# Kernel tuning notes

Measured on AMD Instinct MI355X. Metric: run time of the kernel, lower is better.

Reference implementation:

```python
import jax, jax.numpy as jnp
import numpy as np

S, B, NIN = 64, 64, 64          # att_width (= target_seq_len), batch, num_input
H1, HB, H = 128, 128, 128       # first LSTM size, biLSTM hidden, att_hid
MLP = (1024, 512, 256, 128, 1)  # h1..h4, num_output


def _lstm_cell(x, h, c, Wih, Whh, b):
    # PyTorch gate order: i, f, g, o
    z = x @ Wih.T + h @ Whh.T + b
    i, f, g, o = jnp.split(z, 4, axis=-1)
    c = jax.nn.sigmoid(f) * c + jax.nn.sigmoid(i) * jnp.tanh(g)
    h = jax.nn.sigmoid(o) * jnp.tanh(c)
    return h, c


def _lstm_seq(xs, Wih, Whh, b, reverse=False):
    # xs: [S, B, in] -> hs: [S, B, H], final (h, c)
    h0 = jnp.zeros((xs.shape[1], Whh.shape[1]), xs.dtype)

    def step(carry, x):
        h, c = _lstm_cell(x, carry[0], carry[1], Wih, Whh, b)
        return (h, c), h

    (h, c), hs = jax.lax.scan(step, (h0, h0), xs, reverse=reverse)
    return hs, (h, c)


def _forward(input_seqs,
             lstm1_Wih, lstm1_Whh, lstm1_b,
             bi2f_Wih, bi2f_Whh, bi2f_b, bi2b_Wih, bi2b_Whh, bi2b_b,
             bi3f_Wih, bi3f_Whh, bi3f_b, bi3b_Wih, bi3b_Whh, bi3b_b,
             enc_Wih, enc_Whh, enc_b,
             dec_Wih, dec_Whh, dec_b,
             att_fc_W, att_w,
             W1_W, W1_b, W2_W, W2_b, W3_W, W3_b, W4_W, W4_b, out_W, out_b):
    # 1) one-directional LSTM
    x, _ = _lstm_seq(input_seqs, lstm1_Wih, lstm1_Whh, lstm1_b)
    # 2-3) two stacked bidirectional LSTMs
    f, _ = _lstm_seq(x, bi2f_Wih, bi2f_Whh, bi2f_b)
    bk, _ = _lstm_seq(x, bi2b_Wih, bi2b_Whh, bi2b_b, reverse=True)
    x = jnp.concatenate([f, bk], axis=-1)            # [S,B,2*HB]
    f, _ = _lstm_seq(x, bi3f_Wih, bi3f_Whh, bi3f_b)
    bk, _ = _lstm_seq(x, bi3b_Wih, bi3b_Whh, bi3b_b, reverse=True)
    x = jnp.concatenate([f, bk], axis=-1)            # [S,B,2*HB]
    # 4) encoder LSTM
    enc_out, (eh, ec) = _lstm_seq(x, enc_Wih, enc_Whh, enc_b)  # [S,B,H]
    # per-step attention decode loop (S sequential steps)
    def dec_step(carry, _):
        xin, h, c = carry
        h, c = _lstm_cell(xin, h, c, dec_Wih, dec_Whh, dec_b)   # [B,H]
        # 'concat' attention: tanh(fc(h + enc_out)) @ w -> scores over S
        scores = jnp.tanh((h[None, :, :] + enc_out) @ att_fc_W.T) @ att_w  # [S,B]
        aw = jax.nn.softmax(scores, axis=0)
        ctx = jnp.einsum('sb,sbh->bh', aw, enc_out)             # [B,H]
        out = jnp.concatenate([h, ctx], axis=-1)                # [B,2H]
        return (h, h, c), out

    _, dec_outs = jax.lax.scan(dec_step, (enc_out[-1], eh, ec), None, length=S)
    # [S,B,2H] -> [B, S*2H]
    flat = dec_outs.transpose(1, 0, 2).reshape(dec_outs.shape[1], -1)
    # 5-6) flatten + 4-layer tanh MLP + linear head
    x = jnp.tanh(flat @ W1_W.T + W1_b)
    x = jnp.tanh(x @ W2_W.T + W2_b)
    x = jnp.tanh(x @ W3_W.T + W3_b)
    x = jnp.tanh(x @ W4_W.T + W4_b)
    return x @ out_W.T + out_b


def setup_inputs() -> dict:
    key = jax.random.key(0)
    ks = iter(jax.random.split(key, 40))

    def mat(shape, scale=0.08):
        return (jax.random.normal(next(ks), shape) * scale).astype(jnp.float32)

    d = {}
    d['input_seqs'] = jax.random.normal(next(ks), (S, B, NIN), dtype=jnp.float32)

    def lstm_p(pfx, inp, hid):
        d[pfx + '_Wih'] = mat((4 * hid, inp))
        d[pfx + '_Whh'] = mat((4 * hid, hid))
        d[pfx + '_b'] = mat((4 * hid,))

    lstm_p('lstm1', NIN, H1)
    lstm_p('bi2f', H1, HB); lstm_p('bi2b', H1, HB)
    lstm_p('bi3f', 2 * HB, HB); lstm_p('bi3b', 2 * HB, HB)
    lstm_p('enc', 2 * HB, H)
    lstm_p('dec', H, H)
    d['att_fc_W'] = mat((H, H))
    d['att_w'] = mat((H,))
    dims = [2 * H * S] + list(MLP)
    names = ['W1', 'W2', 'W3', 'W4', 'out']
    for i, nm in enumerate(names):
        d[nm + '_W'] = mat((dims[i + 1], dims[i]))
        d[nm + '_b'] = mat((dims[i + 1],))
    return d


def reference(input_seqs,
              lstm1_Wih, lstm1_Whh, lstm1_b,
              bi2f_Wih, bi2f_Whh, bi2f_b, bi2b_Wih, bi2b_Whh, bi2b_b,
              bi3f_Wih, bi3f_Whh, bi3f_b, bi3b_Wih, bi3b_Whh, bi3b_b,
              enc_Wih, enc_Whh, enc_b,
              dec_Wih, dec_Whh, dec_b,
              att_fc_W, att_w,
              W1_W, W1_b, W2_W, W2_b, W3_W, W3_b, W4_W, W4_b, out_W, out_b):
    return _forward(input_seqs,
                    lstm1_Wih, lstm1_Whh, lstm1_b,
                    bi2f_Wih, bi2f_Whh, bi2f_b, bi2b_Wih, bi2b_Whh, bi2b_b,
                    bi3f_Wih, bi3f_Whh, bi3f_b, bi3b_Wih, bi3b_Whh, bi3b_b,
                    enc_Wih, enc_Whh, enc_b,
                    dec_Wih, dec_Whh, dec_b,
                    att_fc_W, att_w,
                    W1_W, W1_b, W2_W, W2_b, W3_W, W3_b, W4_W, W4_b, out_W, out_b)
```

## Files before the change

kernel.cpp:

```cpp
#include <hip/hip_runtime.h>
#include <hip/hip_bf16.h>

typedef unsigned int u32;
typedef unsigned short u16;

typedef _Float16 half2_t __attribute__((ext_vector_type(2)));
union H2U { u32 u; half2_t h; };

typedef _Float16 f16x8 __attribute__((ext_vector_type(8)));
typedef float f32x4 __attribute__((ext_vector_type(4)));
union F16V { uint4 u; f16x8 h; };

#if defined(__has_builtin)
#if __has_builtin(__builtin_amdgcn_fdot2)
#define HAS_FDOT2 1
#endif
#if __has_builtin(__builtin_amdgcn_update_dpp)
#define HAS_DPP 1
#endif
#endif

__device__ __forceinline__ float bf2f(u32 u) {
  union { u32 i; float f; } v; v.i = u << 16; return v.f;
}
__device__ __forceinline__ float sigf(float x) {
  return 1.0f / (1.0f + __expf(-x));
}
__device__ __forceinline__ float tanhfast(float x) {
  return 2.0f / (1.0f + __expf(-2.0f * x)) - 1.0f;
}
__device__ __forceinline__ u16 f2bf(float f) {
  u32 u = __float_as_uint(f);
  u += 0x7fffu + ((u >> 16) & 1u);
  return (u16)(u >> 16);
}
__device__ __forceinline__ u16 f2h(float f) {
  union { _Float16 h; u16 u; } v; v.h = (_Float16)f; return v.u;
}
__device__ __forceinline__ u32 fpair2h2(float a, float b) {
  H2U r; r.h.x = (_Float16)a; r.h.y = (_Float16)b; return r.u;
}
__device__ __forceinline__ u32 bfpair2h2(u32 two_bf) {
  H2U r;
  r.h.x = (_Float16)bf2f(two_bf & 0xffffu);
  r.h.y = (_Float16)bf2f(two_bf >> 16);
  return r.u;
}
__device__ __forceinline__ float dot2acc(u32 wu, u32 hu, float acc) {
  H2U w, h; w.u = wu; h.u = hu;
#ifdef HAS_FDOT2
  return __builtin_amdgcn_fdot2(w.h, h.h, acc, false);
#else
  acc = fmaf((float)w.h.x, (float)h.h.x, acc);
  return fmaf((float)w.h.y, (float)h.h.y, acc);
#endif
}
template <int CTRL>
__device__ __forceinline__ float dppf(float x) {
#ifdef HAS_DPP
  int y = __builtin_amdgcn_update_dpp(0, __float_as_int(x), CTRL, 0xF, 0xF, true);
  return __int_as_float(y);
#else
  const int lane = threadIdx.x & 63;
  if (CTRL == 0xB1)  return __shfl_xor(x, 1, 64);
  if (CTRL == 0x4E)  return __shfl_xor(x, 2, 64);
  if (CTRL == 0x104) return __shfl_down(x, 4, 64);
  return __shfl(x, (lane & ~3) | (CTRL & 3), 64);
#endif
}

__global__ void k_detect(const u32* __restrict__ w, int* __restrict__ flag) {
  __shared__ int cnt;
  if (threadIdx.x == 0) cnt = 0;
  __syncthreads();
  int c = 0;
  for (int i = threadIdx.x; i < 8192; i += 256) {
    const u32 lo = w[i] & 0xffffu;
    const u32 e = (lo >> 7) & 0xffu;
    c += (e >= 100u && e <= 140u) ? 1 : 0;
  }
  atomicAdd(&cnt, c);
  __syncthreads();
  if (threadIdx.x == 0) *flag = (cnt > 4915) ? 1 : 0;
}

struct Job { const void* s; float* d; int n; int f16; };
struct Jobs { Job j[30]; };

__global__ void k_cvt_all(Jobs J, const int* __restrict__ flag) {
  const Job jb = J.j[blockIdx.y];
  const int isbf = *flag;
  for (int i = blockIdx.x * 256 + threadIdx.x; i < jb.n; i += 32 * 256) {
    const float v = isbf ? bf2f(((const u16*)jb.s)[i]) : ((const float*)jb.s)[i];
    if (jb.f16) ((u16*)jb.d)[i] = f2h(v);
    else        jb.d[i] = v;
  }
}

struct IJobs { const float* b[4]; float* d[4]; int n[4]; int mask[4]; };
__global__ void k_init4(IJobs I) {
  const int j = blockIdx.y;
  const float* bb = I.b[j];
  float* dd = I.d[j];
  const int n = I.n[j], mask = I.mask[j];
  for (int i = blockIdx.x * 256 + threadIdx.x; i < n; i += gridDim.x * 256)
    dd[i] = bb[i & mask];
}

struct PJobs { const float* s[7]; const float* s2[7]; u32* d[7]; };
__global__ void k_pack(PJobs P) {
  const float* src = P.s[blockIdx.y];
  const float* src2 = P.s2[blockIdx.y];
  u32* dst = P.d[blockIdx.y];
  const int i = blockIdx.x * 256 + threadIdx.x;
  const int tid = i >> 6, rem = i & 63;
  const int j = rem >> 4, kk = rem & 15;
  const int r = tid >> 2, kq = tid & 3;
  const int row = r + 128 * j, col = kq * 32 + 2 * kk;
  float v0 = src[row * 128 + col];
  float v1 = src[row * 128 + col + 1];
  if (src2) { v0 += src2[row * 128 + col]; v1 += src2[row * 128 + col + 1]; }
  H2U v;
  v.h.x = (_Float16)v0;
  v.h.y = (_Float16)v1;
  dst[i] = v.u;
}

__launch_bounds__(256)
__global__ void k_mf(const u16* __restrict__ A, int lda,
                     const void* __restrict__ Wv, int ldw,
                     const float* __restrict__ bias,
                     float* __restrict__ C, int ldc,
                     int K, int atom, int wfollow,
                     const int* __restrict__ dflag)
{
  __shared__ __align__(16) u16 As[64][40];
  __shared__ __align__(16) u16 Bs[64][40];
  const int isbf = wfollow ? *dflag : 0;
  const int tid = threadIdx.x;
  const int m0 = blockIdx.x * 64, n0 = blockIdx.y * 64;
  const int kc = K / gridDim.z;
  const int k0 = blockIdx.z * kc;
  const int row = tid >> 2, part = tid & 3;
  const int l = tid & 63, w = tid >> 6;
  const int wr = w >> 1, wc = w & 1;
  const int fr = l & 15, fk = l >> 4;
  f32x4 acc[2][2] = {};
  const u16*   Ap   = A + (size_t)(m0 + row) * lda + k0 + part * 8;
  const u16*   Wp16 = (const u16*)Wv   + (size_t)(n0 + row) * ldw + k0 + part * 8;
  const float* Wp32 = (const float*)Wv + (size_t)(n0 + row) * ldw + k0 + part * 8;

  for (int kk = 0; kk < kc; kk += 32) {
    const uint4 av = *(const uint4*)(Ap + kk);
    uint4 wv;
    if (isbf) {
      const uint4 wu = *(const uint4*)(Wp16 + kk);
      wv.x = bfpair2h2(wu.x); wv.y = bfpair2h2(wu.y);
      wv.z = bfpair2h2(wu.z); wv.w = bfpair2h2(wu.w);
    } else {
      const float4 w0 = *(const float4*)(Wp32 + kk);
      const float4 w1 = *(const float4*)(Wp32 + kk + 4);
      wv.x = fpair2h2(w0.x, w0.y); wv.y = fpair2h2(w0.z, w0.w);
      wv.z = fpair2h2(w1.x, w1.y); wv.w = fpair2h2(w1.z, w1.w);
    }
    __syncthreads();
    *(uint4*)&As[row][part * 8] = av;
    *(uint4*)&Bs[row][part * 8] = wv;
    __syncthreads();
    F16V a0, a1, b0, b1;
    a0.u = *(const uint4*)&As[wr * 32 + fr][fk * 8];
    a1.u = *(const uint4*)&As[wr * 32 + 16 + fr][fk * 8];
    b0.u = *(const uint4*)&Bs[wc * 32 + fr][fk * 8];
    b1.u = *(const uint4*)&Bs[wc * 32 + 16 + fr][fk * 8];
    acc[0][0] = __builtin_amdgcn_mfma_f32_16x16x32_f16(a0.h, b0.h, acc[0][0], 0, 0, 0);
    acc[0][1] = __builtin_amdgcn_mfma_f32_16x16x32_f16(a0.h, b1.h, acc[0][1], 0, 0, 0);
    acc[1][0] = __builtin_amdgcn_mfma_f32_16x16x32_f16(a1.h, b0.h, acc[1][0], 0, 0, 0);
    acc[1][1] = __builtin_amdgcn_mfma_f32_16x16x32_f16(a1.h, b1.h, acc[1][1], 0, 0, 0);
  }

  #pragma unroll
  for (int i = 0; i < 2; ++i) {
    #pragma unroll
    for (int j = 0; j < 2; ++j) {
      const int n = n0 + wc * 32 + j * 16 + fr;
      const float bv = (bias && !atom) ? bias[n] : 0.0f;
      #pragma unroll
      for (int q = 0; q < 4; ++q) {
        const int m = m0 + wr * 32 + i * 16 + fk * 4 + q;
        if (atom) atomicAdd(&C[(size_t)m * ldc + n], acc[i][j][q]);
        else      C[(size_t)m * ldc + n] = acc[i][j][q] + bv;
      }
    }
  }
}

__launch_bounds__(256)
__global__ void k_gemm(const float* __restrict__ A, int lda,
                       const void* __restrict__ Wv, int ldw,
                       const float* __restrict__ bias,
                       float* __restrict__ C, int ldc,
                       int K, int actA, int atom, int wfollow,
                       const int* __restrict__ dflag)
{
  __shared__ float As[32][65];
  __shared__ float Ws[32][65];
  const int isbf = wfollow ? *dflag : 0;
  const int tid = threadIdx.x;
  const int tx = tid & 15, ty = tid >> 4;
  const int m0 = blockIdx.x * 64, n0 = blockIdx.y * 64;
  const int kc = K / gridDim.z;
  const int k0 = blockIdx.z * kc;
  const int lr = tid >> 2;
  const int lk = (tid & 3) << 3;
  float acc[4][4] = {{0.f}};
  const float* Ap   = A + (size_t)(m0 + lr) * lda + k0 + lk;
  const u16*   Wp16 = (const u16*)Wv   + (size_t)(n0 + lr) * ldw + k0 + lk;
  const float* Wp32 = (const float*)Wv + (size_t)(n0 + lr) * ldw + k0 + lk;
  for (int kk = 0; kk < kc; kk += 32) {
    float4 av0 = *(const float4*)(Ap + kk);
    float4 av1 = *(const float4*)(Ap + kk + 4);
    float wv[8];
    if (isbf) {
      const uint4 wu = *(const uint4*)(Wp16 + kk);
      wv[0]=bf2f(wu.x & 0xffffu); wv[1]=bf2f(wu.x >> 16);
      wv[2]=bf2f(wu.y & 0xffffu); wv[3]=bf2f(wu.y >> 16);
      wv[4]=bf2f(wu.z & 0xffffu); wv[5]=bf2f(wu.z >> 16);
      wv[6]=bf2f(wu.w & 0xffffu); wv[7]=bf2f(wu.w >> 16);
    } else {
      const float4 w0 = *(const float4*)(Wp32 + kk);
      const float4 w1 = *(const float4*)(Wp32 + kk + 4);
      wv[0]=w0.x; wv[1]=w0.y; wv[2]=w0.z; wv[3]=w0.w;
      wv[4]=w1.x; wv[5]=w1.y; wv[6]=w1.z; wv[7]=w1.w;
    }
    if (actA) {
      av0.x = tanhfast(av0.x); av0.y = tanhfast(av0.y);
      av0.z = tanhfast(av0.z); av0.w = tanhfast(av0.w);
      av1.x = tanhfast(av1.x); av1.y = tanhfast(av1.y);
      av1.z = tanhfast(av1.z); av1.w = tanhfast(av1.w);
    }
    __syncthreads();
    As[lk+0][lr] = av0.x; As[lk+1][lr] = av0.y;
    As[lk+2][lr] = av0.z; As[lk+3][lr] = av0.w;
    As[lk+4][lr] = av1.x; As[lk+5][lr] = av1.y;
    As[lk+6][lr] = av1.z; As[lk+7][lr] = av1.w;
    #pragma unroll
    for (int q = 0; q < 8; ++q) Ws[lk+q][lr] = wv[q];
    __syncthreads();
    #pragma unroll
    for (int k = 0; k < 32; ++k) {
      float a[4], w[4];
      #pragma unroll
      for (int i = 0; i < 4; ++i) a[i] = As[k][ty + 16*i];
      #pragma unroll
      for (int j = 0; j < 4; ++j) w[j] = Ws[k][tx + 16*j];
      #pragma unroll
      for (int i = 0; i < 4; ++i)
        #pragma unroll
        for (int j = 0; j < 4; ++j)
          acc[i][j] = fmaf(a[i], w[j], acc[i][j]);
    }
  }
  #pragma unroll
  for (int i = 0; i < 4; ++i) {
    const int m = m0 + ty + 16*i;
    #pragma unroll
    for (int j = 0; j < 4; ++j) {
      const int n = n0 + tx + 16*j;
      if (atom) atomicAdd(&C[(size_t)m*ldc + n], acc[i][j]);
      else {
        const float bv = bias ? bias[n] : 0.0f;
        C[(size_t)m*ldc + n] = acc[i][j] + bv;
      }
    }
  }
}

__launch_bounds__(512)
__attribute__((amdgpu_waves_per_eu(2, 2)))
__global__ void k_rec(const float* __restrict__ Zf, const float* __restrict__ Zb,
                      const u32* __restrict__ Wf, const u32* __restrict__ Wb,
                      float* __restrict__ HS, int hstride, int offF, int offB,
                      const float* __restrict__ h0, const float* __restrict__ c0,
                      int zmode, int zld, float* __restrict__ Cout, int hf16)
{
  const int b = blockIdx.x & 63;
  const int dir = blockIdx.x >> 6;
  const float* Z = dir ? Zb : Zf;
  const u32* Wg = dir ? Wb : Wf;
  const int off = dir ? offB : offF;
  const int tid = threadIdx.x;
  const int r = tid >> 2, kq = tid & 3;

  __shared__ __align__(16) float zall[64*512];
  __shared__ __align__(16) u32 hbuf[2][64];

  if (!zmode) {
    #pragma unroll
    for (int q = 0; q < 16; ++q) {
      const int fid = tid + 512*q;
      const int s = fid >> 7, c4 = (fid & 127) << 2;
      const int cs = c4 ^ (((c4 >> 7) & 1) << 4);
      *(float4*)&zall[s*512 + cs] = *(const float4*)&Z[((size_t)s*64 + b)*zld + c4];
    }
  }

  u32 wp[64];
  {
    const uint4* wr = (const uint4*)(Wg + (size_t)tid * 64);
    #pragma unroll
    for (int q = 0; q < 16; ++q) {
      const uint4 u = wr[q];
      wp[q*4+0]=u.x; wp[q*4+1]=u.y; wp[q*4+2]=u.z; wp[q*4+3]=u.w;
    }
  }
  #pragma unroll
  for (int q = 0; q < 64; ++q)
    asm volatile("" : "+v"(wp[q]));

  float creg = c0 ? c0[b*128 + r] : 0.0f;
  if (tid < 64) {
    H2U v;
    if (h0) {
      v.h.x = (_Float16)h0[b*128 + 2*tid];
      v.h.y = (_Float16)h0[b*128 + 2*tid + 1];
    } else {
      v.h.x = (_Float16)0.f; v.h.y = (_Float16)0.f;
    }
    hbuf[0][tid] = v.u;
  }

  const int colz = (r + 128*kq) ^ ((kq & 1) << 4);
  float zdec = 0.f;
  if (zmode) zdec = Z[r + 128*kq];
  const float* zp = zall + (dir ? 63*512 : 0) + colz;
  const int zstep = dir ? -512 : 512;
  size_t hidx = ((size_t)(dir ? 63 : 0)*64 + b)*hstride + off + r;
  const ptrdiff_t hstep = (ptrdiff_t)(dir ? -64 : 64) * hstride;
  const bool beta = (kq & 1) != 0;
  const bool gmm  = (kq & 2) != 0;
  const bool isg  = (kq == 2);
  __syncthreads();

  for (int t = 0; t < 64; ++t) {
    float zcv;
    if (zmode) zcv = zdec;
    else       zcv = *zp;
    u32 hh16[16];
    {
      const u32* hp = hbuf[t & 1];
      *(uint4*)&hh16[0]  = *(const uint4*)&hp[kq*16];
      *(uint4*)&hh16[4]  = *(const uint4*)&hp[kq*16 + 4];
      *(uint4*)&hh16[8]  = *(const uint4*)&hp[kq*16 + 8];
      *(uint4*)&hh16[12] = *(const uint4*)&hp[kq*16 + 12];
    }
    float a[4] = {0.f,0.f,0.f,0.f};
    #pragma unroll
    for (int j = 0; j < 4; ++j)
      #pragma unroll
      for (int i = 0; i < 16; ++i)
        a[j] = dot2acc(wp[j*16 + i], hh16[i], a[j]);
    const float u0 = beta ? a[1] : a[0];
    const float v0 = beta ? a[0] : a[1];
    const float u1 = beta ? a[3] : a[2];
    const float v1 = beta ? a[2] : a[3];
    const float x01 = u0 + dppf<0xB1>(v0);
    const float x23 = u1 + dppf<0xB1>(v1);
    const float keep = gmm ? x23 : x01;
    const float send = gmm ? x01 : x23;
    const float g = keep + dppf<0x4E>(send) + zcv;
    const float s = sigf(isg ? g + g : g);
    const float val = isg ? s + s - 1.0f : s;
    const float si  = dppf<0x00>(val);
    const float sf  = dppf<0x55>(val);
    const float tgg = dppf<0xAA>(val);
    const float so  = dppf<0xFF>(val);
    const float cc = sf * creg + si * tgg;
    const float hh = so * tanhfast(cc);
    creg = cc;
    const float hn = dppf<0x104>(hh);
    if (kq == 0) {
      if (hf16) ((u16*)HS)[hidx] = f2h(hh);
      else      HS[hidx] = hh;
      if (!(r & 1)) {
        H2U v; v.h.x = (_Float16)hh; v.h.y = (_Float16)hn;
        hbuf[(t+1) & 1][r >> 1] = v.u;
      }
    }
    zp += zstep;
    hidx += hstep;
    __syncthreads();
  }

  if (Cout != nullptr && kq == 0) Cout[b*128 + r] = creg;
}

#define TS 132
__launch_bounds__(256, 1)
__global__ void k_att(const float* __restrict__ enco, const float* __restrict__ encp,
                      const float* __restrict__ Hdec, const float* __restrict__ Hproj,
                      const float* __restrict__ attw, u16* __restrict__ flat)
{
  const int b = blockIdx.x;
  const int t0 = blockIdx.y * 16;
  const int tid = threadIdx.x;
  __shared__ __align__(16) float ep[64*TS];
  __shared__ __align__(16) float en[64*TS];
  __shared__ __align__(16) float hp[16*TS];
  __shared__ float S[64*17];
  __shared__ float aw[64*17];
  __shared__ __align__(16) float awt[128];

  for (int i = tid; i < 8192; i += 256) {
    const int s = i >> 7, k = i & 127;
    const size_t g = ((size_t)s*64 + b)*128 + k;
    ep[s*TS + k] = encp[g];
    en[s*TS + k] = enco[g];
  }
  for (int i = tid; i < 2048; i += 256) {
    const int t = i >> 7, k = i & 127;
    const size_t g = ((size_t)(t0 + t)*64 + b)*128 + k;
    hp[t*TS + k] = Hproj[g];
    flat[(size_t)b*16384 + (t0 + t)*256 + k] = f2h(Hdec[g]);
  }
  if (tid < 128) awt[tid] = attw[tid];
  __syncthreads();

  {
    const int t = tid & 15, sg = tid >> 4;
    #pragma unroll
    for (int i = 0; i < 4; ++i) {
      const int s = sg*4 + i;
      float acc = 0.f;
      #pragma unroll 8
      for (int k = 0; k < 128; k += 4) {
        const float4 h4 = *(const float4*)&hp[t*TS + k];
        const float4 e4 = *(const float4*)&ep[s*TS + k];
        const float4 w4 = *(const float4*)&awt[k];
        acc = fmaf(w4.x, tanhfast(h4.x + e4.x), acc);
        acc = fmaf(w4.y, tanhfast(h4.y + e4.y), acc);
        acc = fmaf(w4.z, tanhfast(h4.z + e4.z), acc);
        acc = fmaf(w4.w, tanhfast(h4.w + e4.w), acc);
      }
      S[s*17 + t] = acc;
    }
  }
  __syncthreads();
  if (tid < 16) {
    const int t = tid;
    float m = -1e30f;
    for (int s = 0; s < 64; ++s) m = fmaxf(m, S[s*17 + t]);
    float sum = 0.f;
    for (int s = 0; s < 64; ++s) {
      const float e = __expf(S[s*17 + t] - m);
      aw[s*17 + t] = e;
      sum += e;
    }
    const float inv = 1.0f / sum;
    for (int s = 0; s < 64; ++s) aw[s*17 + t] *= inv;
  }
  __syncthreads();
  {
    const int t = tid >> 4, kg = tid & 15;
    float c0a[8] = {0,0,0,0,0,0,0,0};
    for (int s = 0; s < 64; ++s) {
      const float a = aw[s*17 + t];
      const float4 e0 = *(const float4*)&en[s*TS + kg*8];
      const float4 e1 = *(const float4*)&en[s*TS + kg*8 + 4];
      c0a[0] = fmaf(a, e0.x, c0a[0]);
      c0a[1] = fmaf(a, e0.y, c0a[1]);
      c0a[2] = fmaf(a, e0.z, c0a[2]);
      c0a[3] = fmaf(a, e0.w, c0a[3]);
      c0a[4] = fmaf(a, e1.x, c0a[4]);
      c0a[5] = fmaf(a, e1.y, c0a[5]);
      c0a[6] = fmaf(a, e1.z, c0a[6]);
      c0a[7] = fmaf(a, e1.w, c0a[7]);
    }
    union { u16 s[8]; uint4 u; } o;
    #pragma unroll
    for (int q = 0; q < 8; ++q) o.s[q] = f2h(c0a[q]);
    u16* dst = &flat[(size_t)b*16384 + (t0 + t)*256 + 128 + kg*8];
    *(uint4*)dst = o.u;
  }
}

__global__ void k_head(const float* __restrict__ a4, const float* __restrict__ outW,
                       const float* __restrict__ outb, void* __restrict__ out,
                       const int* __restrict__ dflag)
{
  const int b = threadIdx.x;
  float acc = outb[0];
  #pragma unroll 8
  for (int k = 0; k < 128; ++k)
    acc = fmaf(outW[k], tanhfast(a4[b*128 + k]), acc);
  if (*dflag) ((u16*)out)[b] = f2bf(acc);
  else        ((float*)out)[b] = acc;
}

extern "C" void kernel_launch(void* const* d_in, const int* in_sizes, int n_in,
                              void* d_out, int out_size, void* d_ws, size_t ws_size,
                              hipStream_t stream)
{
  (void)in_sizes; (void)n_in; (void)out_size; (void)ws_size;

  float* p = (float*)d_ws;
  int*   flagp = (int*)p;    p += 64;
  float* x0    = p; p += 64*64*64;
  float* cl1Wih = p; p += 512*64;
  float* cl1Whh = p; p += 512*128;
  float* cl1b   = p; p += 512;
  float* c2Wih  = p; p += 1024*128;
  float* c2bias = p; p += 1024;
  float* c2fWhh = p; p += 512*128;
  float* c2bWhh = p; p += 512*128;
  float* c3Wih  = p; p += 1024*256;
  float* c3bias = p; p += 1024;
  float* c3fWhh = p; p += 512*128;
  float* c3bWhh = p; p += 512*128;
  float* ceWih  = p; p += 512*256;
  float* ceWhh  = p; p += 512*128;
  float* ceb    = p; p += 512;
  float* cdWih  = p; p += 512*128;
  float* cdWhh  = p; p += 512*128;
  float* cdb    = p; p += 512;
  float* cattW  = p; p += 128*128;
  float* cattw  = p; p += 128;
  float* cW1b   = p; p += 1024;
  float* cW2b   = p; p += 512;
  float* cW3b   = p; p += 256;
  float* cW4b   = p; p += 128;
  float* coW    = p; p += 128;
  float* cob    = p; p += 16;
  u32* wpL1 = (u32*)p; p += 32768;
  u32* wp2f = (u32*)p; p += 32768;
  u32* wp2b = (u32*)p; p += 32768;
  u32* wp3f = (u32*)p; p += 32768;
  u32* wp3b = (u32*)p; p += 32768;
  u32* wpE  = (u32*)p; p += 32768;
  u32* wpD  = (u32*)p; p += 32768;
  float* Zf   = p; p += 4096*512;
  float* Z2   = p; p += 4096*1024;
  float* h1   = p; p += 4096*128;
  float* x2   = p; p += 4096*256;
  float* x3   = p; p += 4096*256;
  float* enco = p; p += 4096*128;
  float* Hdec = p; p += 4096*128;
  float* encp = p; p += 4096*128;
  float* Hprj = p; p += 4096*128;
  float* ec   = p; p += 64*128;
  float* flat = p; p += 64*16384;
  float* a1   = p; p += 64*1024;
  float* a2   = p; p += 64*512;
  float* a3   = p; p += 64*256;
  float* a4   = p; p += 64*128;

  k_detect<<<1, 256, 0, stream>>>((const u32*)d_in[2], flagp);

  Jobs J;
  int nj = 0;
  auto add = [&](const void* s, float* d, int n, int f16 = 0) {
    J.j[nj].s = s; J.j[nj].d = d; J.j[nj].n = n; J.j[nj].f16 = f16; ++nj;
  };
  add(d_in[0],  x0,     64*64*64, 1);
  add(d_in[1],  cl1Wih, 512*64);
  add(d_in[2],  cl1Whh, 512*128);
  add(d_in[3],  cl1b,   512);
  add(d_in[4],  c2Wih,            512*128);
  add(d_in[7],  c2Wih + 512*128,  512*128);
  add(d_in[6],  c2bias,       512);
  add(d_in[9],  c2bias + 512, 512);
  add(d_in[5],  c2fWhh, 512*128);
  add(d_in[8],  c2bWhh, 512*128);
  add(d_in[10], c3Wih,            512*256);
  add(d_in[13], c3Wih + 512*256,  512*256);
  add(d_in[12], c3bias,       512);
  add(d_in[15], c3bias + 512, 512);
  add(d_in[11], c3fWhh, 512*128);
  add(d_in[14], c3bWhh, 512*128);
  add(d_in[16], ceWih,  512*256);
  add(d_in[17], ceWhh,  512*128);
  add(d_in[18], ceb,    512);
  add(d_in[19], cdWih,  512*128);
  add(d_in[20], cdWhh,  512*128);
  add(d_in[21], cdb,    512);
  add(d_in[22], cattW,  128*128);
  add(d_in[23], cattw,  128);
  add(d_in[25], cW1b,   1024);
  add(d_in[27], cW2b,   512);
  add(d_in[29], cW3b,   256);
  add(d_in[31], cW4b,   128);
  add(d_in[32], coW,    128);
  add(d_in[33], cob,    1);
  k_cvt_all<<<dim3(32, nj), 256, 0, stream>>>(J, flagp);

  PJobs P;
  for (int i = 0; i < 7; ++i) P.s2[i] = nullptr;
  P.s[0] = cl1Whh; P.d[0] = wpL1;
  P.s[1] = c2fWhh; P.d[1] = wp2f;
  P.s[2] = c2bWhh; P.d[2] = wp2b;
  P.s[3] = c3fWhh; P.d[3] = wp3f;
  P.s[4] = c3bWhh; P.d[4] = wp3b;
  P.s[5] = ceWhh;  P.d[5] = wpE;
  P.s[6] = cdWih;  P.s2[6] = cdWhh; P.d[6] = wpD;
  k_pack<<<dim3(128, 7), 256, 0, stream>>>(P);

  k_mf<<<dim3(64,8,1), 256, 0, stream>>>((const u16*)x0, 64, cl1Wih, 64, cl1b, Zf, 512, 64, 0, 0, flagp);
  k_rec<<<64, 512, 0, stream>>>(Zf, Zf, wpL1, wpL1, h1, 128, 0, 0, nullptr, nullptr, 0, 512, nullptr, 1);

  k_mf<<<dim3(64,16,1), 256, 0, stream>>>((const u16*)h1, 128, c2Wih, 128, c2bias, Z2, 1024, 128, 0, 0, flagp);
  k_rec<<<128, 512, 0, stream>>>(Z2, Z2 + 512, wp2f, wp2b, x2, 256, 0, 128, nullptr, nullptr, 0, 1024, nullptr, 1);

  k_mf<<<dim3(64,16,1), 256, 0, stream>>>((const u16*)x2, 256, c3Wih, 256, c3bias, Z2, 1024, 256, 0, 0, flagp);
  k_rec<<<128, 512, 0, stream>>>(Z2, Z2 + 512, wp3f, wp3b, x3, 256, 0, 128, nullptr, nullptr, 0, 1024, nullptr, 1);

  k_mf<<<dim3(64,8,1), 256, 0, stream>>>((const u16*)x3, 256, ceWih, 256, ceb, Zf, 512, 256, 0, 0, flagp);
  k_rec<<<64, 512, 0, stream>>>(Zf, Zf, wpE, wpE, enco, 128, 0, 0, nullptr, nullptr, 0, 512, ec, 0);

  k_rec<<<64, 512, 0, stream>>>(cdb, cdb, wpD, wpD, Hdec, 128, 0, 0,
                                enco + (size_t)63*64*128, ec, 1, 512, nullptr, 0);

  k_gemm<<<dim3(128,2,1), 256, 0, stream>>>(enco, 128, cattW, 128, nullptr, encp, 128, 128, 0, 0, 0, flagp);

  k_att<<<dim3(64,4), 256, 0, stream>>>(enco, encp, Hdec, Hprj, cattw, (u16*)flat);

  IJobs I;
  I.b[0]=cW1b; I.d[0]=a1; I.n[0]=64*1024; I.mask[0]=1023;
  I.b[1]=cW2b; I.d[1]=a2; I.n[1]=64*512;  I.mask[1]=511;
  I.b[2]=cW3b; I.d[2]=a3; I.n[2]=64*256;  I.mask[2]=255;
  I.b[3]=cW4b; I.d[3]=a4; I.n[3]=64*128;  I.mask[3]=127;
  k_init4<<<dim3(64, 4), 256, 0, stream>>>(I);
  k_mf<<<dim3(1,16,64), 256, 0, stream>>>((const u16*)flat, 16384, d_in[24], 16384, nullptr, a1, 1024, 16384, 1, 1, flagp);
  k_gemm<<<dim3(1,8,16), 256, 0, stream>>>(a1, 1024, d_in[26], 1024, nullptr, a2, 512, 1024, 1, 1, 1, flagp);
  k_gemm<<<dim3(1,4,8), 256, 0, stream>>>(a2, 512, d_in[28], 512, nullptr, a3, 256, 512, 1, 1, 1, flagp);
  k_gemm<<<dim3(1,2,4), 256, 0, stream>>>(a3, 256, d_in[30], 256, nullptr, a4, 128, 256, 1, 1, 1, flagp);

  k_head<<<1, 64, 0, stream>>>(a4, coW, cob, d_out, flagp);
}
```

Measured before the change: 547.8 us.

## Merge prep kernels, replace atomic split-K MLP with partial-sum reduction and fused MFMA tanh

The conversion and packing kernels are merged into one launch, and the recurrent weights are now packed straight from the raw inputs instead of being converted first. The first MLP layer now writes 16 split-K partial tiles that a new reduction kernel sums, then adds bias and tanh and stores fp16. This replaces the bias-init kernel and the atomics. The remaining MLP layers run on the MFMA GEMM with bias+tanh in the epilogue, emitting fp16 activations for the next layer and the head. This cuts launches, atomics and fp32 traffic, at the cost of fewer blocks in the small GEMMs and fp16 rounding of activations.

Result: slower. 587.3 us (+7.2%).

```diff
diff --git a/kernel.cpp b/kernel.cpp
--- a/kernel.cpp
+++ b/kernel.cpp
@@ -37,6 +37,9 @@
 __device__ __forceinline__ u16 f2h(float f) {
   union { _Float16 h; u16 u; } v; v.h = (_Float16)f; return v.u;
 }
+__device__ __forceinline__ float h2f(u16 u) {
+  union { u16 u; _Float16 h; } v; v.u = u; return (float)v.h;
+}
 __device__ __forceinline__ u32 fpair2h2(float a, float b) {
   H2U r; r.h.x = (_Float16)a; r.h.y = (_Float16)b; return r.u;
 }
@@ -45,6 +48,9 @@
   r.h.x = (_Float16)bf2f(two_bf & 0xffffu);
   r.h.y = (_Float16)bf2f(two_bf >> 16);
   return r.u;
+}
+__device__ __forceinline__ float ldf(const void* p, int idx, int isbf) {
+  return isbf ? bf2f(((const u16*)p)[idx]) : ((const float*)p)[idx];
 }
 __device__ __forceinline__ float dot2acc(u32 wu, u32 hu, float acc) {
   H2U w, h; w.u = wu; h.u = hu;
@@ -85,45 +91,40 @@
 }
 
 struct Job { const void* s; float* d; int n; int f16; };
-struct Jobs { Job j[30]; };
-
-__global__ void k_cvt_all(Jobs J, const int* __restrict__ flag) {
-  const Job jb = J.j[blockIdx.y];
+struct Jobs { Job j[24]; int nj; };
+struct PJobs { const void* s[7]; const void* s2[7]; u32* d[7]; };
+
+__global__ void k_prep(Jobs J, PJobs P, const int* __restrict__ flag) {
   const int isbf = *flag;
-  for (int i = blockIdx.x * 256 + threadIdx.x; i < jb.n; i += 32 * 256) {
-    const float v = isbf ? bf2f(((const u16*)jb.s)[i]) : ((const float*)jb.s)[i];
-    if (jb.f16) ((u16*)jb.d)[i] = f2h(v);
-    else        jb.d[i] = v;
-  }
-}
-
-struct IJobs { const float* b[4]; float* d[4]; int n[4]; int mask[4]; };
-__global__ void k_init4(IJobs I) {
-  const int j = blockIdx.y;
-  const float* bb = I.b[j];
-  float* dd = I.d[j];
-  const int n = I.n[j], mask = I.mask[j];
-  for (int i = blockIdx.x * 256 + threadIdx.x; i < n; i += gridDim.x * 256)
-    dd[i] = bb[i & mask];
-}
-
-struct PJobs { const float* s[7]; const float* s2[7]; u32* d[7]; };
-__global__ void k_pack(PJobs P) {
-  const float* src = P.s[blockIdx.y];
-  const float* src2 = P.s2[blockIdx.y];
-  u32* dst = P.d[blockIdx.y];
-  const int i = blockIdx.x * 256 + threadIdx.x;
-  const int tid = i >> 6, rem = i & 63;
-  const int j = rem >> 4, kk = rem & 15;
-  const int r = tid >> 2, kq = tid & 3;
-  const int row = r + 128 * j, col = kq * 32 + 2 * kk;
-  float v0 = src[row * 128 + col];
-  float v1 = src[row * 128 + col + 1];
-  if (src2) { v0 += src2[row * 128 + col]; v1 += src2[row * 128 + col + 1]; }
-  H2U v;
-  v.h.x = (_Float16)v0;
-  v.h.y = (_Float16)v1;
-  dst[i] = v.u;
+  const int y = blockIdx.y;
+  if (y < J.nj) {
+    const Job jb = J.j[y];
+    for (int i = blockIdx.x * 256 + threadIdx.x; i < jb.n; i += gridDim.x * 256) {
+      const float v = ldf(jb.s, i, isbf);
+      if (jb.f16) ((u16*)jb.d)[i] = f2h(v);
+      else        jb.d[i] = v;
+    }
+  } else {
+    const int py = y - J.nj;
+    const void* src = P.s[py];
+    const void* src2 = P.s2[py];
+    u32* dst = P.d[py];
+    const int i = blockIdx.x * 256 + threadIdx.x;
+    const int tid = i >> 6, rem = i & 63;
+    const int j = rem >> 4, kk = rem & 15;
+    const int r = tid >> 2, kq = tid & 3;
+    const int row = r + 128 * j, col = kq * 32 + 2 * kk;
+    float v0 = ldf(src, row * 128 + col, isbf);
+    float v1 = ldf(src, row * 128 + col + 1, isbf);
+    if (src2) {
+      v0 += ldf(src2, row * 128 + col, isbf);
+      v1 += ldf(src2, row * 128 + col + 1, isbf);
+    }
+    H2U v;
+    v.h.x = (_Float16)v0;
+    v.h.y = (_Float16)v1;
+    dst[i] = v.u;
+  }
 }
 
 __launch_bounds__(256)
@@ -131,7 +132,7 @@
                      const void* __restrict__ Wv, int ldw,
                      const float* __restrict__ bias,
                      float* __restrict__ C, int ldc,
-                     int K, int atom, int wfollow,
+                     int K, int emode, int pstride, int wfollow,
                      const int* __restrict__ dflag)
 {
   __shared__ __align__(16) u16 As[64][40];
@@ -178,20 +179,31 @@
     acc[1][1] = __builtin_amdgcn_mfma_f32_16x16x32_f16(a1.h, b1.h, acc[1][1], 0, 0, 0);
   }
 
+  float* Cp = (emode == 3) ? (C + (size_t)blockIdx.z * pstride) : C;
   #pragma unroll
   for (int i = 0; i < 2; ++i) {
     #pragma unroll
     for (int j = 0; j < 2; ++j) {
       const int n = n0 + wc * 32 + j * 16 + fr;
-      const float bv = (bias && !atom) ? bias[n] : 0.0f;
+      const float bv = (bias && emode != 3) ? bias[n] : 0.0f;
       #pragma unroll
       for (int q = 0; q < 4; ++q) {
         const int m = m0 + wr * 32 + i * 16 + fk * 4 + q;
-        if (atom) atomicAdd(&C[(size_t)m * ldc + n], acc[i][j][q]);
-        else      C[(size_t)m * ldc + n] = acc[i][j][q] + bv;
+        if (emode == 2)      ((u16*)C)[(size_t)m * ldc + n] = f2h(tanhfast(acc[i][j][q] + bv));
+        else if (emode == 3) Cp[(size_t)m * ldc + n] = acc[i][j][q];
+        else                 C[(size_t)m * ldc + n] = acc[i][j][q] + bv;
       }
     }
   }
+}
+
+__global__ void k_red(const float* __restrict__ p, const float* __restrict__ b,
+                      u16* __restrict__ o) {
+  const int i = blockIdx.x * 256 + threadIdx.x;
+  float s = 0.f;
+  #pragma unroll
+  for (int z = 0; z < 16; ++z) s += p[z * 65536 + i];
+  o[i] = f2h(tanhfast(s + b[i & 1023]));
 }
 
 __launch_bounds__(256)
@@ -483,7 +495,7 @@
   }
 }
 
-__global__ void k_head(const float* __restrict__ a4, const float* __restrict__ outW,
+__global__ void k_head(const u16* __restrict__ a4, const float* __restrict__ outW,
                        const float* __restrict__ outb, void* __restrict__ out,
                        const int* __restrict__ dflag)
 {
@@ -491,7 +503,7 @@
   float acc = outb[0];
   #pragma unroll 8
   for (int k = 0; k < 128; ++k)
-    acc = fmaf(outW[k], tanhfast(a4[b*128 + k]), acc);
+    acc = fmaf(outW[k], h2f(a4[b*128 + k]), acc);
   if (*dflag) ((u16*)out)[b] = f2bf(acc);
   else        ((float*)out)[b] = acc;
 }
@@ -506,21 +518,13 @@
   int*   flagp = (int*)p;    p += 64;
   float* x0    = p; p += 64*64*64;
   float* cl1Wih = p; p += 512*64;
-  float* cl1Whh = p; p += 512*128;
   float* cl1b   = p; p += 512;
   float* c2Wih  = p; p += 1024*128;
   float* c2bias = p; p += 1024;
-  float* c2fWhh = p; p += 512*128;
-  float* c2bWhh = p; p += 512*128;
   float* c3Wih  = p; p += 1024*256;
   float* c3bias = p; p += 1024;
-  float* c3fWhh = p; p += 512*128;
-  float* c3bWhh = p; p += 512*128;
   float* ceWih  = p; p += 512*256;
-  float* ceWhh  = p; p += 512*128;
   float* ceb    = p; p += 512;
-  float* cdWih  = p; p += 512*128;
-  float* cdWhh  = p; p += 512*128;
   float* cdb    = p; p += 512;
   float* cattW  = p; p += 128*128;
   float* cattw  = p; p += 128;
@@ -548,10 +552,11 @@
   float* Hprj = p; p += 4096*128;
   float* ec   = p; p += 64*128;
   float* flat = p; p += 64*16384;
-  float* a1   = p; p += 64*1024;
-  float* a2   = p; p += 64*512;
-  float* a3   = p; p += 64*256;
-  float* a4   = p; p += 64*128;
+  float* a1p  = p; p += 16*64*1024;
+  float* a1t  = p; p += 32768;
+  float* a2t  = p; p += 16384;
+  float* a3t  = p; p += 8192;
+  float* a4t  = p; p += 4096;
 
   k_detect<<<1, 256, 0, stream>>>((const u32*)d_in[2], flagp);
 
@@ -562,25 +567,17 @@
   };
   add(d_in[0],  x0,     64*64*64, 1);
   add(d_in[1],  cl1Wih, 512*64);
-  add(d_in[2],  cl1Whh, 512*128);
   add(d_in[3],  cl1b,   512);
   add(d_in[4],  c2Wih,            512*128);
   add(d_in[7],  c2Wih + 512*128,  512*128);
   add(d_in[6],  c2bias,       512);
   add(d_in[9],  c2bias + 512, 512);
-  add(d_in[5],  c2fWhh, 512*128);
-  add(d_in[8],  c2bWhh, 512*128);
   add(d_in[10], c3Wih,            512*256);
   add(d_in[13], c3Wih + 512*256,  512*256);
   add(d_in[12], c3bias,       512);
   add(d_in[15], c3bias + 512, 512);
-  add(d_in[11], c3fWhh, 512*128);
-  add(d_in[14], c3bWhh, 512*128);
   add(d_in[16], ceWih,  512*256);
-  add(d_in[17], ceWhh,  512*128);
   add(d_in[18], ceb,    512);
-  add(d_in[19], cdWih,  512*128);
-  add(d_in[20], cdWhh,  512*128);
   add(d_in[21], cdb,    512);
   add(d_in[22], cattW,  128*128);
   add(d_in[23], cattw,  128);
@@ -590,29 +587,28 @@
   add(d_in[31], cW4b,   128);
   add(d_in[32], coW,    128);
   add(d_in[33], cob,    1);
-  k_cvt_all<<<dim3(32, nj), 256, 0, stream>>>(J, flagp);
-
+  J.nj = nj;
   PJobs P;
   for (int i = 0; i < 7; ++i) P.s2[i] = nullptr;
-  P.s[0] = cl1Whh; P.d[0] = wpL1;
-  P.s[1] = c2fWhh; P.d[1] = wp2f;
-  P.s[2] = c2bWhh; P.d[2] = wp2b;
-  P.s[3] = c3fWhh; P.d[3] = wp3f;
-  P.s[4] = c3bWhh; P.d[4] = wp3b;
-  P.s[5] = ceWhh;  P.d[5] = wpE;
-  P.s[6] = cdWih;  P.s2[6] = cdWhh; P.d[6] = wpD;
-  k_pack<<<dim3(128, 7), 256, 0, stream>>>(P);
-
-  k_mf<<<dim3(64,8,1), 256, 0, stream>>>((const u16*)x0, 64, cl1Wih, 64, cl1b, Zf, 512, 64, 0, 0, flagp);
+  P.s[0] = d_in[2];  P.d[0] = wpL1;
+  P.s[1] = d_in[5];  P.d[1] = wp2f;
+  P.s[2] = d_in[8];  P.d[2] = wp2b;
+  P.s[3] = d_in[11]; P.d[3] = wp3f;
+  P.s[4] = d_in[14]; P.d[4] = wp3b;
+  P.s[5] = d_in[17]; P.d[5] = wpE;
+  P.s[6] = d_in[19]; P.s2[6] = d_in[20]; P.d[6] = wpD;
+  k_prep<<<dim3(128, nj + 7), 256, 0, stream>>>(J, P, flagp);
+
+  k_mf<<<dim3(64,8,1), 256, 0, stream>>>((const u16*)x0, 64, cl1Wih, 64, cl1b, Zf, 512, 64, 0, 0, 0, flagp);
   k_rec<<<64, 512, 0, stream>>>(Zf, Zf, wpL1, wpL1, h1, 128, 0, 0, nullptr, nullptr, 0, 512, nullptr, 1);
 
-  k_mf<<<dim3(64,16,1), 256, 0, stream>>>((const u16*)h1, 128, c2Wih, 128, c2bias, Z2, 1024, 128, 0, 0, flagp);
+  k_mf<<<dim3(64,16,1), 256, 0, stream>>>((const u16*)h1, 128, c2Wih, 128, c2bias, Z2, 1024, 128, 0, 0, 0, flagp);
   k_rec<<<128, 512, 0, stream>>>(Z2, Z2 + 512, wp2f, wp2b, x2, 256, 0, 128, nullptr, nullptr, 0, 1024, nullptr, 1);
 
-  k_mf<<<dim3(64,16,1), 256, 0, stream>>>((const u16*)x2, 256, c3Wih, 256, c3bias, Z2, 1024, 256, 0, 0, flagp);
+  k_mf<<<dim3(64,16,1), 256, 0, stream>>>((const u16*)x2, 256, c3Wih, 256, c3bias, Z2, 1024, 256, 0, 0, 0, flagp);
   k_rec<<<128, 512, 0, stream>>>(Z2, Z2 + 512, wp3f, wp3b, x3, 256, 0, 128, nullptr, nullptr, 0, 1024, nullptr, 1);
 
-  k_mf<<<dim3(64,8,1), 256, 0, stream>>>((const u16*)x3, 256, ceWih, 256, ceb, Zf, 512, 256, 0, 0, flagp);
+  k_mf<<<dim3(64,8,1), 256, 0, stream>>>((const u16*)x3, 256, ceWih, 256, ceb, Zf, 512, 256, 0, 0, 0, flagp);
   k_rec<<<64, 512, 0, stream>>>(Zf, Zf, wpE, wpE, enco, 128, 0, 0, nullptr, nullptr, 0, 512, ec, 0);
 
   k_rec<<<64, 512, 0, stream>>>(cdb, cdb, wpD, wpD, Hdec, 128, 0, 0,
@@ -622,16 +618,11 @@
 
   k_att<<<dim3(64,4), 256, 0, stream>>>(enco, encp, Hdec, Hprj, cattw, (u16*)flat);
 
-  IJobs I;
-  I.b[0]=cW1b; I.d[0]=a1; I.n[0]=64*1024; I.mask[0]=1023;
-  I.b[1]=cW2b; I.d[1]=a2; I.n[1]=64*512;  I.mask[1]=511;
-  I.b[2]=cW3b; I.d[2]=a3; I.n[2]=64*256;  I.mask[2]=255;
-  I.b[3]=cW4b; I.d[3]=a4; I.n[3]=64*128;  I.mask[3]=127;
-  k_init4<<<dim3(64, 4), 256, 0, stream>>>(I);
-  k_mf<<<dim3(1,16,64), 256, 0, stream>>>((const u16*)flat, 16384, d_in[24], 16384, nullptr, a1, 1024, 16384, 1, 1, flagp);
-  k_gemm<<<dim3(1,8,16), 256, 0, stream>>>(a1, 1024, d_in[26], 1024, nullptr, a2, 512, 1024, 1, 1, 1, flagp);
-  k_gemm<<<dim3(1,4,8), 256, 0, stream>>>(a2, 512, d_in[28], 512, nullptr, a3, 256, 512, 1, 1, 1, flagp);
-  k_gemm<<<dim3(1,2,4), 256, 0, stream>>>(a3, 256, d_in[30], 256, nullptr, a4, 128, 256, 1, 1, 1, flagp);
-
-  k_head<<<1, 64, 0, stream>>>(a4, coW, cob, d_out, flagp);
-}
+  k_mf<<<dim3(1,16,16), 256, 0, stream>>>((const u16*)flat, 16384, d_in[24], 16384, nullptr, a1p, 1024, 16384, 3, 65536, 1, flagp);
+  k_red<<<256, 256, 0, stream>>>(a1p, cW1b, (u16*)a1t);
+  k_mf<<<dim3(1,8,1), 256, 0, stream>>>((const u16*)a1t, 1024, d_in[26], 1024, cW2b, a2t, 512, 1024, 2, 0, 1, flagp);
+  k_mf<<<dim3(1,4,1), 256, 0, stream>>>((const u16*)a2t, 512, d_in[28], 512, cW3b, a3t, 256, 512, 2, 0, 1, flagp);
+  k_mf<<<dim3(1,2,1), 256, 0, stream>>>((const u16*)a3t, 256, d_in[30], 256, cW4b, a4t, 128, 256, 2, 0, 1, flagp);
+
+  k_head<<<1, 64, 0, stream>>>((const u16*)a4t, coW, cob, d_out, flagp);
+}
```

## Fuse MLP layers 2-4 and output head into one per-batch tail kernel

Applied to the files above, without the earlier changes.

Replaces the three split-K GEMM launches for MLP layers 2-4 and the separate head kernel with a single kernel: one block per batch row keeps the activations in shared memory and computes each layer as per-thread dot products. This removes three launches, the intermediate global buffers, and the init of their accumulators. In exchange, each block reads all W2/W3/W4 weights separately, about 64x redundant weight traffic mostly served from cache. The per-thread row-strided dot products may have poor memory coalescing and less parallelism than the split-K GEMMs.

Result: slower. 607.6 us (+10.9%).

```diff
diff --git a/kernel.cpp b/kernel.cpp
--- a/kernel.cpp
+++ b/kernel.cpp
@@ -483,17 +483,130 @@
   }
 }
 
-__global__ void k_head(const float* __restrict__ a4, const float* __restrict__ outW,
-                       const float* __restrict__ outb, void* __restrict__ out,
-                       const int* __restrict__ dflag)
+__launch_bounds__(256)
+__global__ void k_tail(const float* __restrict__ a1,
+                       const void* __restrict__ W2v, const float* __restrict__ b2,
+                       const void* __restrict__ W3v, const float* __restrict__ b3,
+                       const void* __restrict__ W4v, const float* __restrict__ b4,
+                       const float* __restrict__ oW, const float* __restrict__ ob,
+                       void* __restrict__ out, const int* __restrict__ dflag)
 {
-  const int b = threadIdx.x;
-  float acc = outb[0];
-  #pragma unroll 8
-  for (int k = 0; k < 128; ++k)
-    acc = fmaf(outW[k], tanhfast(a4[b*128 + k]), acc);
-  if (*dflag) ((u16*)out)[b] = f2bf(acc);
-  else        ((float*)out)[b] = acc;
+  const int b = blockIdx.x;
+  const int tid = threadIdx.x;
+  const int isbf = *dflag;
+  __shared__ float h2[1024];
+  __shared__ float h3[512];
+  __shared__ float h4[128];
+  __shared__ float red[256];
+
+  {
+    const float4 v = *(const float4*)&a1[(size_t)b*1024 + tid*4];
+    h2[tid*4+0] = tanhfast(v.x); h2[tid*4+1] = tanhfast(v.y);
+    h2[tid*4+2] = tanhfast(v.z); h2[tid*4+3] = tanhfast(v.w);
+  }
+  __syncthreads();
+
+  #pragma unroll
+  for (int jj = 0; jj < 2; ++jj) {
+    const int j = tid*2 + jj;
+    float acc = b2[j];
+    if (isbf) {
+      const u16* w = (const u16*)W2v + (size_t)j*1024;
+      for (int k = 0; k < 1024; k += 8) {
+        const uint4 wu = *(const uint4*)(w + k);
+        acc = fmaf(bf2f(wu.x & 0xffffu), h2[k+0], acc);
+        acc = fmaf(bf2f(wu.x >> 16),     h2[k+1], acc);
+        acc = fmaf(bf2f(wu.y & 0xffffu), h2[k+2], acc);
+        acc = fmaf(bf2f(wu.y >> 16),     h2[k+3], acc);
+        acc = fmaf(bf2f(wu.z & 0xffffu), h2[k+4], acc);
+        acc = fmaf(bf2f(wu.z >> 16),     h2[k+5], acc);
+        acc = fmaf(bf2f(wu.w & 0xffffu), h2[k+6], acc);
+        acc = fmaf(bf2f(wu.w >> 16),     h2[k+7], acc);
+      }
+    } else {
+      const float* w = (const float*)W2v + (size_t)j*1024;
+      for (int k = 0; k < 1024; k += 4) {
+        const float4 wv = *(const float4*)(w + k);
+        acc = fmaf(wv.x, h2[k+0], acc);
+        acc = fmaf(wv.y, h2[k+1], acc);
+        acc = fmaf(wv.z, h2[k+2], acc);
+        acc = fmaf(wv.w, h2[k+3], acc);
+      }
+    }
+    h3[j] = tanhfast(acc);
+  }
+  __syncthreads();
+
+  {
+    const int j = tid;
+    float acc = b3[j];
+    if (isbf) {
+      const u16* w = (const u16*)W3v + (size_t)j*512;
+      for (int k = 0; k < 512; k += 8) {
+        const uint4 wu = *(const uint4*)(w + k);
+        acc = fmaf(bf2f(wu.x & 0xffffu), h3[k+0], acc);
+        acc = fmaf(bf2f(wu.x >> 16),     h3[k+1], acc);
+        acc = fmaf(bf2f(wu.y & 0xffffu), h3[k+2], acc);
+        acc = fmaf(bf2f(wu.y >> 16),     h3[k+3], acc);
+        acc = fmaf(bf2f(wu.z & 0xffffu), h3[k+4], acc);
+        acc = fmaf(bf2f(wu.z >> 16),     h3[k+5], acc);
+        acc = fmaf(bf2f(wu.w & 0xffffu), h3[k+6], acc);
+        acc = fmaf(bf2f(wu.w >> 16),     h3[k+7], acc);
+      }
+    } else {
+      const float* w = (const float*)W3v + (size_t)j*512;
+      for (int k = 0; k < 512; k += 4) {
+        const float4 wv = *(const float4*)(w + k);
+        acc = fmaf(wv.x, h3[k+0], acc);
+        acc = fmaf(wv.y, h3[k+1], acc);
+        acc = fmaf(wv.z, h3[k+2], acc);
+        acc = fmaf(wv.w, h3[k+3], acc);
+      }
+    }
+    red[tid] = tanhfast(acc);
+  }
+  __syncthreads();
+  if (tid < 128) {
+    const int j = tid;
+    float acc = b4[j];
+    if (isbf) {
+      const u16* w = (const u16*)W4v + (size_t)j*256;
+      for (int k = 0; k < 256; k += 8) {
+        const uint4 wu = *(const uint4*)(w + k);
+        acc = fmaf(bf2f(wu.x & 0xffffu), red[k+0], acc);
+        acc = fmaf(bf2f(wu.x >> 16),     red[k+1], acc);
+        acc = fmaf(bf2f(wu.y & 0xffffu), red[k+2], acc);
+        acc = fmaf(bf2f(wu.y >> 16),     red[k+3], acc);
+        acc = fmaf(bf2f(wu.z & 0xffffu), red[k+4], acc);
+        acc = fmaf(bf2f(wu.z >> 16),     red[k+5], acc);
+        acc = fmaf(bf2f(wu.w & 0xffffu), red[k+6], acc);
+        acc = fmaf(bf2f(wu.w >> 16),     red[k+7], acc);
+      }
+    } else {
+      const float* w = (const float*)W4v + (size_t)j*256;
+      for (int k = 0; k < 256; k += 4) {
+        const float4 wv = *(const float4*)(w + k);
+        acc = fmaf(wv.x, red[k+0], acc);
+        acc = fmaf(wv.y, red[k+1], acc);
+        acc = fmaf(wv.z, red[k+2], acc);
+        acc = fmaf(wv.w, red[k+3], acc);
+      }
+    }
+    h4[j] = tanhfast(acc);
+  }
+  __syncthreads();
+  float pp = (tid < 128) ? oW[tid] * h4[tid] : 0.0f;
+  red[tid] = pp;
+  __syncthreads();
+  for (int st = 128; st > 0; st >>= 1) {
+    if (tid < st) red[tid] += red[tid + st];
+    __syncthreads();
+  }
+  if (tid == 0) {
+    const float acc = red[0] + ob[0];
+    if (isbf) ((u16*)out)[b] = f2bf(acc);
+    else      ((float*)out)[b] = acc;
+  }
 }
 
 extern "C" void kernel_launch(void* const* d_in, const int* in_sizes, int n_in,
@@ -549,9 +662,6 @@
   float* ec   = p; p += 64*128;
   float* flat = p; p += 64*16384;
   float* a1   = p; p += 64*1024;
-  float* a2   = p; p += 64*512;
-  float* a3   = p; p += 64*256;
-  float* a4   = p; p += 64*128;
 
   k_detect<<<1, 256, 0, stream>>>((const u32*)d_in[2], flagp);
 
@@ -624,14 +734,11 @@
 
   IJobs I;
   I.b[0]=cW1b; I.d[0]=a1; I.n[0]=64*1024; I.mask[0]=1023;
-  I.b[1]=cW2b; I.d[1]=a2; I.n[1]=64*512;  I.mask[1]=511;
-  I.b[2]=cW3b; I.d[2]=a3; I.n[2]=64*256;  I.mask[2]=255;
-  I.b[3]=cW4b; I.d[3]=a4; I.n[3]=64*128;  I.mask[3]=127;
-  k_init4<<<dim3(64, 4), 256, 0, stream>>>(I);
+  I.b[1]=cW1b; I.d[1]=a1; I.n[1]=0; I.mask[1]=0;
+  I.b[2]=cW1b; I.d[2]=a1; I.n[2]=0; I.mask[2]=0;
+  I.b[3]=cW1b; I.d[3]=a1; I.n[3]=0; I.mask[3]=0;
+  k_init4<<<dim3(64, 1), 256, 0, stream>>>(I);
   k_mf<<<dim3(1,16,64), 256, 0, stream>>>((const u16*)flat, 16384, d_in[24], 16384, nullptr, a1, 1024, 16384, 1, 1, flagp);
-  k_gemm<<<dim3(1,8,16), 256, 0, stream>>>(a1, 1024, d_in[26], 1024, nullptr, a2, 512, 1024, 1, 1, 1, flagp);
-  k_gemm<<<dim3(1,4,8), 256, 0, stream>>>(a2, 512, d_in[28], 512, nullptr, a3, 256, 512, 1, 1, 1, flagp);
-  k_gemm<<<dim3(1,2,4), 256, 0, stream>>>(a3, 256, d_in[30], 256, nullptr, a4, 128, 256, 1, 1, 1, flagp);
-
-  k_head<<<1, 64, 0, stream>>>(a4, coW, cob, d_out, flagp);
-}
+  k_tail<<<64, 256, 0, stream>>>(a1, d_in[26], cW2b, d_in[28], cW3b,
+                                 d_in[30], cW4b, coW, cob, d_out, flagp);
+}
```
